# Optimization experiments

Measured on AMD Instinct MI355X. Metric: run time of the kernel, lower is better.

The kernel has to match this reference:

```python
import jax, jax.numpy as jnp
import numpy as np
import math
from jax import lax

B, HS, WS, C, T, TD, HH, TOPM = 8, 64, 64, 512, 77, 512, 8, 3
DH = C // HH
CONF_TH = 0.35


def _layernorm(x, w, b, eps=1e-5):
    mu = x.mean(-1, keepdims=True)
    var = ((x - mu) ** 2).mean(-1, keepdims=True)
    return (x - mu) * lax.rsqrt(var + eps) * w + b


def _l2norm(x, eps=1e-6):
    n = jnp.sqrt((x * x).sum(-1, keepdims=True))
    return x / jnp.maximum(n, eps)


def _forward(visual_features, text_features, geo_mask,
             ln1_w, ln1_b, wq, bq, wk, bk, wv, bv, wo, bo,
             gate_w, gate_b, logit_scale, alpha,
             ln2_w, ln2_b, ffn_w1, ffn_b1, ffn_w2, ffn_b2):
    Bb, Hs, Ws, Cv = visual_features.shape
    N = Hs * Ws
    # Pre-LN + flatten spatial
    x = _layernorm(visual_features, ln1_w, ln1_b).reshape(Bb, N, Cv)
    q_full = x @ wq + bq                                  # [B,N,C]
    pad_mask = jnp.abs(text_features).sum(-1) <= 1e-6     # [B,T]
    k_full = text_features @ wk + bk                      # [B,T,C]
    v_full = text_features @ wv + bv
    # per-token L2 normalize over full channel dim, then split heads
    q = _l2norm(q_full).reshape(Bb, N, HH, DH)
    k = _l2norm(k_full).reshape(Bb, T, HH, DH)
    v = v_full.reshape(Bb, T, HH, DH)
    scale = jnp.exp(jnp.clip(logit_scale, -2.0, 2.0)) / jnp.sqrt(jnp.float32(DH))
    sim = jnp.einsum('bnhd,bthd->bnht', q, k) * scale     # [B,N,H,T]
    # geo gate (4D tensor branch): log-bias on logits + multiplicative channel gate later
    gate_map = jnp.clip(geo_mask, 0.3, 1.0)               # [B,1,Hs,Ws]
    geo_gate_flat = gate_map.reshape(Bb, N, 1)            # [B,N,1]
    sim = sim + jnp.log(jnp.maximum(gate_map.reshape(Bb, N), 1e-6))[:, :, None, None]
    sim = jnp.where(pad_mask[:, None, None, :], -jnp.inf, sim)
    # Top-K sparsification before softmax (threshold at the K-th value)
    topv = lax.top_k(sim, TOPM)[0]                        # [B,N,H,K]
    sim = jnp.where(sim >= topv[..., -1:], sim, -jnp.inf)
    attn = jax.nn.softmax(sim, axis=-1)
    attn = attn / jnp.maximum(attn.sum(-1, keepdims=True), 1e-6)
    # fully-padded rows -> zero
    all_pad = pad_mask.all(axis=1)
    attn = jnp.where(all_pad[:, None, None, None], 0.0, attn)
    # confidence bypass: conf = max_prob * (1 - normalized entropy), mean over heads
    a_hn = attn.transpose(0, 2, 1, 3)                     # [B,H,N,T]
    maxp = a_hn.max(-1, keepdims=True)
    t_eff = jnp.maximum((a_hn > 0).astype(a_hn.dtype).sum(-1, keepdims=True), 2.0)
    p = jnp.maximum(a_hn, 1e-8)
    ent = jnp.maximum(-(p * jnp.log(p)).sum(-1, keepdims=True) / jnp.log(t_eff), 0.0)
    conf = jnp.clip(maxp * (1.0 - ent), 0.0, 1.0).mean(axis=1)   # [B,N,1]
    conf_scale = CONF_TH + (1.0 - CONF_TH) * jnp.clip(conf, 0.0, 1.0)
    aligned = jnp.einsum('bnht,bthd->bnhd', attn, v).reshape(Bb, N, HH * DH)
    aligned = (aligned @ wo + bo) * conf_scale
    gate = jax.nn.sigmoid(x @ gate_w + gate_b) * geo_gate_flat
    y = x + alpha * gate * aligned
    h = _layernorm(y, ln2_w, ln2_b)
    y = y + (jax.nn.gelu(h @ ffn_w1 + ffn_b1, approximate=False) @ ffn_w2 + ffn_b2)
    return y.reshape(Bb, Hs, Ws, Cv)


def setup_inputs() -> dict:
    key = jax.random.key(0)
    ks = jax.random.split(key, 16)
    def w(k, shp, fan_in):
        return (jax.random.normal(k, shp, jnp.float32) * (1.0 / math.sqrt(fan_in))).astype(jnp.float32)
    return {
        'visual_features': jax.random.normal(ks[0], (B, HS, WS, C), jnp.float32),
        'text_features':   jax.random.normal(ks[1], (B, T, TD), jnp.float32),
        'geo_mask':        jax.random.uniform(ks[2], (B, 1, HS, WS), jnp.float32),
        'ln1_w': jnp.ones((C,), jnp.float32), 'ln1_b': jnp.zeros((C,), jnp.float32),
        'wq': w(ks[3], (C, C), C),   'bq': jnp.zeros((C,), jnp.float32),
        'wk': w(ks[4], (TD, C), TD), 'bk': jnp.zeros((C,), jnp.float32),
        'wv': w(ks[5], (TD, C), TD), 'bv': jnp.zeros((C,), jnp.float32),
        'wo': w(ks[6], (C, C), C),   'bo': jnp.zeros((C,), jnp.float32),
        'gate_w': w(ks[7], (C, C), C), 'gate_b': jnp.zeros((C,), jnp.float32),
        'logit_scale': jnp.float32(math.log(1.0 / 0.07)),
        'alpha': jnp.float32(0.1),
        'ln2_w': jnp.ones((C,), jnp.float32), 'ln2_b': jnp.zeros((C,), jnp.float32),
        'ffn_w1': w(ks[8], (C, 4 * C), C),    'ffn_b1': jnp.zeros((4 * C,), jnp.float32),
        'ffn_w2': w(ks[9], (4 * C, C), 4 * C), 'ffn_b2': jnp.zeros((C,), jnp.float32),
    }


def reference(visual_features, text_features, geo_mask,
              ln1_w, ln1_b, wq, bq, wk, bk, wv, bv, wo, bo,
              gate_w, gate_b, logit_scale, alpha,
              ln2_w, ln2_b, ffn_w1, ffn_b1, ffn_w2, ffn_b2):
    return _forward(visual_features, text_features, geo_mask,
                    ln1_w, ln1_b, wq, bq, wk, bk, wv, bv, wo, bo,
                    gate_w, gate_b, logit_scale, alpha,
                    ln2_w, ln2_b, ffn_w1, ffn_b1, ffn_w2, ffn_b2)
```

## Files before the change

### kernel.cpp

```cpp
#include <hip/hip_runtime.h>
#include <hip/hip_bf16.h>
#include <math.h>

#define TT 77
#define MTOT 32768

typedef __attribute__((ext_vector_type(8))) short bf16x8;
typedef __attribute__((ext_vector_type(4))) float floatx4;

#define GPTR(p) ((const __attribute__((address_space(1))) void*)(p))
#define LPTR(p) ((__attribute__((address_space(3))) void*)(p))

__device__ __forceinline__ float wred_sum(float v) {
#pragma unroll
  for (int o = 32; o >= 1; o >>= 1) v += __shfl_xor(v, o, 64);
  return v;
}

__device__ __forceinline__ unsigned short f2bf(float f) {
  unsigned int u = __float_as_uint(f);
  unsigned int r = (u + 0x7fffu + ((u >> 16) & 1u)) >> 16;
  return (unsigned short)r;
}
__device__ __forceinline__ float bf2f(unsigned short h) {
  return __uint_as_float(((unsigned int)h) << 16);
}
__device__ __forceinline__ unsigned int cvt2bf(float a, float b) {
  unsigned int r;
  asm("v_cvt_pk_bf16_f32 %0, %1, %2" : "=v"(r) : "v"(a), "v"(b));
  return r;
}

__device__ __forceinline__ float fast_gelu(float o) {
  const float z = fabsf(o) * 0.70710678118654752f;
  const float t = __builtin_amdgcn_rcpf(fmaf(0.3275911f, z, 1.0f));
  float p = fmaf(1.061405429f, t, -1.453152027f);
  p = fmaf(p, t, 1.421413741f);
  p = fmaf(p, t, -0.284496736f);
  p = fmaf(p, t, 0.254829592f);
  p = p * t;
  const float erfz = fmaf(-p, __expf(-z * z), 1.0f);
  const float s = __builtin_copysignf(erfz, o);
  return 0.5f * o * (1.0f + s);
}

__device__ __forceinline__ float fast_sigmoid(float o) {
  return __builtin_amdgcn_rcpf(1.0f + __expf(-o));
}

__global__ __launch_bounds__(256)
void ln_bf16_kernel(const float* __restrict__ in, const float* __restrict__ gw,
                    const float* __restrict__ gb, unsigned short* __restrict__ out) {
  const int wv = threadIdx.x >> 6, lane = threadIdx.x & 63;
  const size_t row = (size_t)blockIdx.x * 4 + wv;
  const float* p = in + row * 512 + lane * 8;
  float4 a = *(const float4*)p;
  float4 b = *(const float4*)(p + 4);
  float s = a.x + a.y + a.z + a.w + b.x + b.y + b.z + b.w;
  float mu = wred_sum(s) * (1.0f / 512.0f);
  float d[8] = {a.x - mu, a.y - mu, a.z - mu, a.w - mu,
                b.x - mu, b.y - mu, b.z - mu, b.w - mu};
  float ss = 0.f;
#pragma unroll
  for (int i = 0; i < 8; ++i) ss = fmaf(d[i], d[i], ss);
  float var = wred_sum(ss) * (1.0f / 512.0f);
  float rstd = rsqrtf(var + 1e-5f);
  float4 w0 = *(const float4*)(gw + lane * 8);
  float4 w1 = *(const float4*)(gw + lane * 8 + 4);
  float4 c0 = *(const float4*)(gb + lane * 8);
  float4 c1 = *(const float4*)(gb + lane * 8 + 4);
  float o[8];
  o[0] = d[0] * rstd * w0.x + c0.x;  o[1] = d[1] * rstd * w0.y + c0.y;
  o[2] = d[2] * rstd * w0.z + c0.z;  o[3] = d[3] * rstd * w0.w + c0.w;
  o[4] = d[4] * rstd * w1.x + c1.x;  o[5] = d[5] * rstd * w1.y + c1.y;
  o[6] = d[6] * rstd * w1.z + c1.z;  o[7] = d[7] * rstd * w1.w + c1.w;
  __align__(16) unsigned short ob[8];
#pragma unroll
  for (int i = 0; i < 8; ++i) ob[i] = f2bf(o[i]);
  *(uint4*)(out + row * 512 + lane * 8) = *(const uint4*)ob;
}

__global__ __launch_bounds__(256)
void zero_ss_kernel(float* __restrict__ ssq) {
  ssq[blockIdx.x * 256 + threadIdx.x] = 0.0f;
}

__global__ __launch_bounds__(256)
void transpose_bf16_kernel(const float* __restrict__ W, unsigned short* __restrict__ WTb,
                           int K, int N) {
  __shared__ float s[32][33];
  const int tx = threadIdx.x & 31, ty = threadIdx.x >> 5;
  const int n0 = blockIdx.x * 32, k0 = blockIdx.y * 32;
#pragma unroll
  for (int j = 0; j < 4; ++j)
    s[ty + 8 * j][tx] = W[(size_t)(k0 + ty + 8 * j) * N + n0 + tx];
  __syncthreads();
#pragma unroll
  for (int j = 0; j < 4; ++j)
    WTb[(size_t)(n0 + ty + 8 * j) * K + k0 + tx] = f2bf(s[tx][ty + 8 * j]);
}

__global__ __launch_bounds__(256)
void transpose_pair_kernel(const float* __restrict__ W,
                           unsigned short* __restrict__ WTh,
                           unsigned short* __restrict__ WTl, int K, int N) {
  __shared__ float s[32][33];
  const int tx = threadIdx.x & 31, ty = threadIdx.x >> 5;
  const int n0 = blockIdx.x * 32, k0 = blockIdx.y * 32;
#pragma unroll
  for (int j = 0; j < 4; ++j)
    s[ty + 8 * j][tx] = W[(size_t)(k0 + ty + 8 * j) * N + n0 + tx];
  __syncthreads();
#pragma unroll
  for (int j = 0; j < 4; ++j) {
    const float a = s[tx][ty + 8 * j];
    const unsigned short hi = f2bf(a);
    WTh[(size_t)(n0 + ty + 8 * j) * K + k0 + tx] = hi;
    WTl[(size_t)(n0 + ty + 8 * j) * K + k0 + tx] = f2bf(a - bf2f(hi));
  }
}

__global__ __launch_bounds__(256)
void text_cvt_kernel(const float* __restrict__ text,
                     unsigned short* __restrict__ thi,
                     unsigned short* __restrict__ tlo,
                     float* __restrict__ negm) {
  const int wv = threadIdx.x >> 6, lane = threadIdx.x & 63;
  const int row = blockIdx.x * 4 + wv;
  if (row >= 616) {
    const uint4 z = {0u, 0u, 0u, 0u};
    *(uint4*)(thi + (size_t)row * 512 + lane * 8) = z;
    *(uint4*)(tlo + (size_t)row * 512 + lane * 8) = z;
    return;
  }
  const float* p = text + (size_t)row * 512 + lane * 8;
  float4 a = *(const float4*)p;
  float4 b = *(const float4*)(p + 4);
  float v[8] = {a.x, a.y, a.z, a.w, b.x, b.y, b.z, b.w};
  float ab = 0.f;
#pragma unroll
  for (int i = 0; i < 8; ++i) ab += fabsf(v[i]);
  ab = wred_sum(ab);
  __align__(16) unsigned short hb[8];
  __align__(16) unsigned short lb[8];
#pragma unroll
  for (int i = 0; i < 8; ++i) {
    hb[i] = f2bf(v[i]);
    lb[i] = f2bf(v[i] - bf2f(hb[i]));
  }
  *(uint4*)(thi + (size_t)row * 512 + lane * 8) = *(const uint4*)hb;
  *(uint4*)(tlo + (size_t)row * 512 + lane * 8) = *(const uint4*)lb;
  if (lane == 0) {
    const int bb = row / 77, t = row - bb * 77;
    negm[bb * 80 + t] = (ab <= 1e-6f) ? -INFINITY : 0.0f;
  }
}

__global__ __launch_bounds__(256)
void kv_gemm(const unsigned short* __restrict__ AH,
             const unsigned short* __restrict__ AL,
             const unsigned short* __restrict__ BH,
             const unsigned short* __restrict__ BL,
             const float* __restrict__ bk, const float* __restrict__ bv,
             float* __restrict__ outp) {
  const int K = 512;
  __shared__ __align__(16) unsigned short AsH[128 * 32];
  __shared__ __align__(16) unsigned short AsL[128 * 32];
  __shared__ __align__(16) unsigned short BsH[128 * 32];
  __shared__ __align__(16) unsigned short BsL[128 * 32];
  const int tid = threadIdx.x;
  const int wid = tid >> 6, lane = tid & 63;
  const int wr = wid >> 1, wc = wid & 1;
  const int m16 = lane & 15, quad = lane >> 4;
  const int row0 = blockIdx.y * 128, col0 = blockIdx.x * 128;

  const floatx4 zero4 = {0.f, 0.f, 0.f, 0.f};
  floatx4 acc[4][4];
#pragma unroll
  for (int i = 0; i < 4; ++i)
#pragma unroll
    for (int j = 0; j < 4; ++j) acc[i][j] = zero4;

  const int srow = tid >> 2;
  const int schunk = (tid & 3) ^ (srow & 3);
  const unsigned short* AgH = AH + (size_t)(row0 + srow) * K + schunk * 8;
  const unsigned short* AgL = AL + (size_t)(row0 + srow) * K + schunk * 8;
  const unsigned short* BgH = BH + (size_t)(col0 + srow) * K + schunk * 8;
  const unsigned short* BgL = BL + (size_t)(col0 + srow) * K + schunk * 8;
  char* AsHB = (char*)AsH + tid * 16;
  char* AsLB = (char*)AsL + tid * 16;
  char* BsHB = (char*)BsH + tid * 16;
  char* BsLB = (char*)BsL + tid * 16;
  const int rq = quad ^ (m16 & 3);
  const int aOfs = (wr * 64 + m16) * 32 + rq * 8;
  const int bOfs = (wc * 64 + m16) * 32 + rq * 8;

  for (int k0 = 0; k0 < K; k0 += 32) {
    __syncthreads();
    __builtin_amdgcn_global_load_lds(GPTR(AgH + k0), LPTR(AsHB), 16, 0, 0);
    __builtin_amdgcn_global_load_lds(GPTR(AgH + (size_t)64 * K + k0), LPTR(AsHB + 4096), 16, 0, 0);
    __builtin_amdgcn_global_load_lds(GPTR(AgL + k0), LPTR(AsLB), 16, 0, 0);
    __builtin_amdgcn_global_load_lds(GPTR(AgL + (size_t)64 * K + k0), LPTR(AsLB + 4096), 16, 0, 0);
    __builtin_amdgcn_global_load_lds(GPTR(BgH + k0), LPTR(BsHB), 16, 0, 0);
    __builtin_amdgcn_global_load_lds(GPTR(BgH + (size_t)64 * K + k0), LPTR(BsHB + 4096), 16, 0, 0);
    __builtin_amdgcn_global_load_lds(GPTR(BgL + k0), LPTR(BsLB), 16, 0, 0);
    __builtin_amdgcn_global_load_lds(GPTR(BgL + (size_t)64 * K + k0), LPTR(BsLB + 4096), 16, 0, 0);
    __syncthreads();
    bf16x8 afH[4], afL[4], bfH[4], bfL[4];
#pragma unroll
    for (int i = 0; i < 4; ++i) {
      afH[i] = *(const bf16x8*)(AsH + aOfs + i * 16 * 32);
      afL[i] = *(const bf16x8*)(AsL + aOfs + i * 16 * 32);
      bfH[i] = *(const bf16x8*)(BsH + bOfs + i * 16 * 32);
      bfL[i] = *(const bf16x8*)(BsL + bOfs + i * 16 * 32);
    }
#pragma unroll
    for (int mi = 0; mi < 4; ++mi)
#pragma unroll
      for (int ni = 0; ni < 4; ++ni) {
        acc[mi][ni] = __builtin_amdgcn_mfma_f32_16x16x32_bf16(afH[mi], bfH[ni], acc[mi][ni], 0, 0, 0);
        acc[mi][ni] = __builtin_amdgcn_mfma_f32_16x16x32_bf16(afH[mi], bfL[ni], acc[mi][ni], 0, 0, 0);
        acc[mi][ni] = __builtin_amdgcn_mfma_f32_16x16x32_bf16(afL[mi], bfH[ni], acc[mi][ni], 0, 0, 0);
      }
  }

  const float* bp = (col0 < 512) ? bk : bv;
  const int cbase = (col0 < 512) ? col0 : col0 - 512;
  float bb[4];
#pragma unroll
  for (int ni = 0; ni < 4; ++ni) bb[ni] = bp[cbase + wc * 64 + ni * 16 + m16];
#pragma unroll
  for (int mi = 0; mi < 4; ++mi)
#pragma unroll
    for (int r = 0; r < 4; ++r) {
      const int row = row0 + wr * 64 + mi * 16 + quad * 4 + r;
#pragma unroll
      for (int ni = 0; ni < 4; ++ni) {
        const int col = col0 + wc * 64 + ni * 16 + m16;
        outp[(size_t)row * 1024 + col] = acc[mi][ni][r] + bb[ni];
      }
    }
}

__global__ __launch_bounds__(256)
void knorm_kernel(const float* __restrict__ KV,
                  unsigned short* __restrict__ khb) {
  const int wv = threadIdx.x >> 6, lane = threadIdx.x & 63;
  const int row = blockIdx.x * 4 + wv;
  const float* p = KV + (size_t)row * 1024 + lane * 8;
  float4 a = *(const float4*)p;
  float4 b = *(const float4*)(p + 4);
  float v[8] = {a.x, a.y, a.z, a.w, b.x, b.y, b.z, b.w};
  float ss = 0.f;
#pragma unroll
  for (int i = 0; i < 8; ++i) ss = fmaf(v[i], v[i], ss);
  ss = wred_sum(ss);
  const float sc = 1.0f / fmaxf(sqrtf(ss), 1e-6f);
  const int bb = row / 77, t = row - bb * 77;
  const int c = lane * 8, h = c >> 6, d = c & 63;
  __align__(16) unsigned short ob[8];
#pragma unroll
  for (int i = 0; i < 8; ++i) ob[i] = f2bf(v[i] * sc);
  *(uint4*)(khb + (((size_t)bb * 8 + h) * 80 + t) * 64 + d) = *(const uint4*)ob;
}

__global__ __launch_bounds__(256)
void kpad_zero_kernel(unsigned short* __restrict__ khb, float* __restrict__ negm) {
  const int i = blockIdx.x * 256 + threadIdx.x;
  const int bh = i / 192, rem = i - bh * 192;
  const int t = 77 + rem / 64, d = rem & 63;
  khb[(((size_t)bh) * 80 + t) * 64 + d] = 0;
  if (i < 24) negm[(i / 3) * 80 + 77 + (i % 3)] = -INFINITY;
}

__global__ __launch_bounds__(256)
void sim_kernel(const unsigned short* __restrict__ qnb,
                const unsigned short* __restrict__ khb,
                const float* __restrict__ negm,
                const float* __restrict__ ssq,
                const float* __restrict__ logit_scale,
                float* __restrict__ SIM) {
  __shared__ __align__(16) unsigned short As[128 * 72];
  __shared__ __align__(16) unsigned short Bs[80 * 72];
  const int bh = blockIdx.y;
  const int b = bh >> 3, h = bh & 7;
  const int row0 = blockIdx.x * 128;
  const int tid = threadIdx.x;
  {
    const int r = tid >> 1, half = tid & 1;
    const unsigned short* src = qnb + ((size_t)b * 4096 + row0 + r) * 512 + h * 64 + half * 32;
    unsigned short* dst = As + r * 72 + half * 32;
    *(uint4*)dst = *(const uint4*)src;
    *(uint4*)(dst + 8) = *(const uint4*)(src + 8);
    *(uint4*)(dst + 16) = *(const uint4*)(src + 16);
    *(uint4*)(dst + 24) = *(const uint4*)(src + 24);
  }
  if (tid < 160) {
    const int r = tid >> 1, half = tid & 1;
    const unsigned short* src = khb + ((size_t)bh * 80 + r) * 64 + half * 32;
    unsigned short* dst = Bs + r * 72 + half * 32;
    *(uint4*)dst = *(const uint4*)src;
    *(uint4*)(dst + 8) = *(const uint4*)(src + 8);
    *(uint4*)(dst + 16) = *(const uint4*)(src + 16);
    *(uint4*)(dst + 24) = *(const uint4*)(src + 24);
  }
  __syncthreads();
  const int w = tid >> 6, lane = tid & 63;
  const int m16 = lane & 15, quad = lane >> 4;
  const unsigned short* aBase = As + (w * 32 + m16) * 72 + quad * 8;
  const unsigned short* bBase = Bs + m16 * 72 + quad * 8;
  bf16x8 af[2][2], bf[5][2];
#pragma unroll
  for (int mi = 0; mi < 2; ++mi)
#pragma unroll
    for (int kk = 0; kk < 2; ++kk)
      af[mi][kk] = *(const bf16x8*)(aBase + mi * 16 * 72 + kk * 32);
#pragma unroll
  for (int ni = 0; ni < 5; ++ni)
#pragma unroll
    for (int kk = 0; kk < 2; ++kk)
      bf[ni][kk] = *(const bf16x8*)(bBase + ni * 16 * 72 + kk * 32);
  const floatx4 zero4 = {0.f, 0.f, 0.f, 0.f};
  floatx4 acc[2][5];
#pragma unroll
  for (int mi = 0; mi < 2; ++mi)
#pragma unroll
    for (int ni = 0; ni < 5; ++ni) acc[mi][ni] = zero4;
#pragma unroll
  for (int kk = 0; kk < 2; ++kk)
#pragma unroll
    for (int mi = 0; mi < 2; ++mi)
#pragma unroll
      for (int ni = 0; ni < 5; ++ni)
        acc[mi][ni] = __builtin_amdgcn_mfma_f32_16x16x32_bf16(af[mi][kk], bf[ni][kk], acc[mi][ni], 0, 0, 0);
  const float ls = fminf(fmaxf(logit_scale[0], -2.0f), 2.0f);
  const float scale = expf(ls) * 0.125f;
  float nm[5];
#pragma unroll
  for (int ni = 0; ni < 5; ++ni) nm[ni] = negm[b * 80 + ni * 16 + m16];
  float* obase = SIM + ((size_t)b * 4096 + row0 + w * 32 + quad * 4) * 640 + h * 4 + (m16 & 3);
  const int jb = m16 >> 2;
#pragma unroll
  for (int mi = 0; mi < 2; ++mi)
#pragma unroll
    for (int r = 0; r < 4; ++r) {
      const int rl = row0 + w * 32 + quad * 4 + mi * 16 + r;
      const float ssv = ssq[(size_t)b * 4096 + rl];
      const float nsc = scale / fmaxf(sqrtf(ssv), 1e-6f);
#pragma unroll
      for (int ni = 0; ni < 5; ++ni)
        obase[(size_t)(mi * 16 + r) * 640 + (ni * 4 + jb) * 32] = acc[mi][ni][r] * nsc + nm[ni];
    }
}

__global__ __launch_bounds__(256)
void attn_topk_pv_kernel(const float* __restrict__ SIM,
                         const float* __restrict__ vf,
                         unsigned short* __restrict__ alignedb,
                         float* __restrict__ conf_out) {
  const int g = blockIdx.x * 256 + threadIdx.x;
  const int b = g >> 15;
  const int local = g & 32767;
  const int n = local >> 3, h = local & 7;
  const float* sp = SIM + ((size_t)b * 4096 + n) * 640 + h * 4;

  float m1 = -INFINITY, m2 = -INFINITY, m3 = -INFINITY, m4 = -INFINITY;
  int a1 = 0, a2 = 0, a3 = 0;
#pragma unroll
  for (int i = 0; i < 20; ++i) {
    const float4 q = *(const float4*)(sp + i * 32);
#pragma unroll
    for (int j = 0; j < 4; ++j) {
      const float v = (j == 0) ? q.x : (j == 1) ? q.y : (j == 2) ? q.z : q.w;
      const int t = i * 4 + j;
      const bool c1 = v > m1, c2 = v > m2, c3 = v > m3, c4 = v > m4;
      m4 = c4 ? (c3 ? m3 : v) : m4;
      m3 = c3 ? (c2 ? m2 : v) : m3;
      a3 = c3 ? (c2 ? a2 : t) : a3;
      m2 = c2 ? (c1 ? m1 : v) : m2;
      a2 = c2 ? (c1 ? a1 : t) : a2;
      m1 = c1 ? v : m1;
      a1 = c1 ? t : a1;
    }
  }

  const bool dead = (m1 == -INFINITY);
  if (dead) m1 = 0.0f;
  const bool tie = (!dead) && ((m1 == m2) || (m2 == m3) || (m3 == m4));

  const float d2 = m2 - m1, d3 = m3 - m1;
  const float e2 = __expf(d2), e3 = __expf(d3);
  float s0 = 1.0f + e2 + e3;
  float s1 = ((e2 > 0.f) ? e2 * d2 : 0.f) + ((e3 > 0.f) ? e3 * d3 : 0.f);
  float cntf = 1.0f + ((e2 > 0.f) ? 1.f : 0.f) + ((e3 > 0.f) ? 1.f : 0.f);

  unsigned short* op = alignedb + ((size_t)b * 4096 + n) * 512 + h * 64;

  if (__any(tie)) {
    if (tie) {
      s0 = 0.f; s1 = 0.f; cntf = 0.f;
      float4 acc[16];
#pragma unroll
      for (int i = 0; i < 16; ++i) acc[i] = (float4){0.f, 0.f, 0.f, 0.f};
      for (int t = 0; t < 80; ++t) {
        const float v = sp[(t >> 2) * 32 + (t & 3)];
        if (v >= m3) {
          const float e = expf(v - m1);
          if (e > 0.f) {
            s0 += e; s1 = fmaf(e, v - m1, s1); cntf += 1.f;
            const float4* vp = (const float4*)(vf + (size_t)(b * 77 + t) * 1024 + h * 64);
#pragma unroll
            for (int i = 0; i < 16; ++i) {
              const float4 x = vp[i];
              acc[i].x = fmaf(e, x.x, acc[i].x);
              acc[i].y = fmaf(e, x.y, acc[i].y);
              acc[i].z = fmaf(e, x.z, acc[i].z);
              acc[i].w = fmaf(e, x.w, acc[i].w);
            }
          }
        }
      }
      const float invt = 1.0f / s0;
#pragma unroll
      for (int i = 0; i < 8; ++i) {
        const float4 lo = acc[2 * i], hi = acc[2 * i + 1];
        uint4 pk;
        pk.x = cvt2bf(lo.x * invt, lo.y * invt);
        pk.y = cvt2bf(lo.z * invt, lo.w * invt);
        pk.z = cvt2bf(hi.x * invt, hi.y * invt);
        pk.w = cvt2bf(hi.z * invt, hi.w * invt);
        *(uint4*)(op + i * 8) = pk;
      }
    }
  }

  const float inv = 1.0f / s0;
  const float entn = (__logf(s0) - s1 * inv) + (77.0f - cntf) * 1.8420681e-7f;
  const float ent = fmaxf(entn / __logf(fmaxf(cntf, 2.0f)), 0.0f);
  float conf_h = fminf(fmaxf(inv * (1.0f - ent), 0.0f), 1.0f);
  if (dead) conf_h = 0.f;
  float cs = conf_h;
  cs += __shfl_xor(cs, 1, 64);
  cs += __shfl_xor(cs, 2, 64);
  cs += __shfl_xor(cs, 4, 64);
  if (h == 0) {
    const float cm = fminf(fmaxf(cs * 0.125f, 0.0f), 1.0f);
    conf_out[(size_t)b * 4096 + n] = 0.35f + 0.65f * cm;
  }

  if (!tie) {
    const float wA = dead ? 0.f : inv;
    const float wB = e2 * inv, wC = e3 * inv;
    const float* v1p = vf + (size_t)(b * 77 + a1) * 1024 + h * 64;
    const float* v2p = vf + (size_t)(b * 77 + a2) * 1024 + h * 64;
    const float* v3p = vf + (size_t)(b * 77 + a3) * 1024 + h * 64;
#pragma unroll
    for (int i = 0; i < 8; ++i) {
      const float4 a0 = ((const float4*)v1p)[2 * i];
      const float4 a1v = ((const float4*)v1p)[2 * i + 1];
      const float4 b0 = ((const float4*)v2p)[2 * i];
      const float4 b1 = ((const float4*)v2p)[2 * i + 1];
      const float4 c0 = ((const float4*)v3p)[2 * i];
      const float4 c1 = ((const float4*)v3p)[2 * i + 1];
      float4 r0, r1;
      r0.x = fmaf(wC, c0.x, fmaf(wB, b0.x, wA * a0.x));
      r0.y = fmaf(wC, c0.y, fmaf(wB, b0.y, wA * a0.y));
      r0.z = fmaf(wC, c0.z, fmaf(wB, b0.z, wA * a0.z));
      r0.w = fmaf(wC, c0.w, fmaf(wB, b0.w, wA * a0.w));
      r1.x = fmaf(wC, c1.x, fmaf(wB, b1.x, wA * a1v.x));
      r1.y = fmaf(wC, c1.y, fmaf(wB, b1.y, wA * a1v.y));
      r1.z = fmaf(wC, c1.z, fmaf(wB, b1.z, wA * a1v.z));
      r1.w = fmaf(wC, c1.w, fmaf(wB, b1.w, wA * a1v.w));
      uint4 pk;
      pk.x = cvt2bf(r0.x, r0.y);
      pk.y = cvt2bf(r0.z, r0.w);
      pk.z = cvt2bf(r1.x, r1.y);
      pk.w = cvt2bf(r1.z, r1.w);
      *(uint4*)(op + i * 8) = pk;
    }
  }
}

template <int EPI, int KC>
__global__ __launch_bounds__(256)
void mfma_gemm(const unsigned short* __restrict__ A,
               const unsigned short* __restrict__ WT,
               const float* __restrict__ bias,
               void* __restrict__ outv, int M, int N,
               const unsigned short* __restrict__ e0b,
               const float* __restrict__ e1f,
               const float* __restrict__ e2f,
               const float* __restrict__ scf) {
  __shared__ __align__(16) unsigned short As[128 * 32];
  __shared__ __align__(16) unsigned short Bs[128 * 32];
  const int tid = threadIdx.x;
  const int wid = tid >> 6, lane = tid & 63;
  const int wr = wid >> 1, wc = wid & 1;
  const int m16 = lane & 15, quad = lane >> 4;

  const int nwg = gridDim.x * gridDim.y;
  const int orig = blockIdx.y * gridDim.x + blockIdx.x;
  const int qq = nwg >> 3, rr = nwg & 7;
  const int xcd = orig & 7, base = orig >> 3;
  const int logical = (xcd < rr ? xcd * (qq + 1) : rr * (qq + 1) + (xcd - rr) * qq) + base;
  const int bx = logical % gridDim.x, by = logical / gridDim.x;
  const int row0 = by * 128, col0 = bx * 128;

  const floatx4 zero4 = {0.f, 0.f, 0.f, 0.f};
  floatx4 acc[4][4];
#pragma unroll
  for (int i = 0; i < 4; ++i)
#pragma unroll
    for (int j = 0; j < 4; ++j) acc[i][j] = zero4;

  const int srow = tid >> 2;
  const int schunk = (tid & 3) ^ (srow & 3);
  const unsigned short* Ag = A + (size_t)(row0 + srow) * KC + schunk * 8;
  const unsigned short* Bg = WT + (size_t)(col0 + srow) * KC + schunk * 8;
  char* AsB = (char*)As + tid * 16;
  char* BsB = (char*)Bs + tid * 16;
  const int rq = quad ^ (m16 & 3);
  const unsigned short* aP = As + (wr * 64 + m16) * 32 + rq * 8;
  const unsigned short* bP = Bs + (wc * 64 + m16) * 32 + rq * 8;

  for (int k0 = 0; k0 < KC; k0 += 32) {
    __syncthreads();
    __builtin_amdgcn_global_load_lds(GPTR(Ag + k0), LPTR(AsB), 16, 0, 0);
    __builtin_amdgcn_global_load_lds(GPTR(Ag + (size_t)64 * KC + k0), LPTR(AsB + 4096), 16, 0, 0);
    __builtin_amdgcn_global_load_lds(GPTR(Bg + k0), LPTR(BsB), 16, 0, 0);
    __builtin_amdgcn_global_load_lds(GPTR(Bg + (size_t)64 * KC + k0), LPTR(BsB + 4096), 16, 0, 0);
    __syncthreads();
    bf16x8 af[4], bfr[4];
#pragma unroll
    for (int i = 0; i < 4; ++i) {
      af[i] = *(const bf16x8*)(aP + i * 16 * 32);
      bfr[i] = *(const bf16x8*)(bP + i * 16 * 32);
    }
#pragma unroll
    for (int mi = 0; mi < 4; ++mi)
#pragma unroll
      for (int ni = 0; ni < 4; ++ni)
        acc[mi][ni] = __builtin_amdgcn_mfma_f32_16x16x32_bf16(af[mi], bfr[ni], acc[mi][ni], 0, 0, 0);
  }

  float* outf = (float*)outv;
  unsigned short* outb = (unsigned short*)outv;
  const unsigned short* albf = (const unsigned short*)e1f;
  float bb[4];
#pragma unroll
  for (int ni = 0; ni < 4; ++ni) bb[ni] = bias[col0 + wc * 64 + ni * 16 + m16];
  const float alphav = (EPI == 2) ? scf[0] : 0.f;

#pragma unroll
  for (int mi = 0; mi < 4; ++mi) {
#pragma unroll
    for (int r = 0; r < 4; ++r) {
      const int row = row0 + wr * 64 + mi * 16 + quad * 4 + r;
      float o[4];
#pragma unroll
      for (int ni = 0; ni < 4; ++ni) o[ni] = acc[mi][ni][r] + bb[ni];
      const size_t basei = (size_t)row * N + col0 + wc * 64 + m16;

      if (EPI == 5) {
        const unsigned int p01 = cvt2bf(o[0], o[1]);
        const unsigned int p23 = cvt2bf(o[2], o[3]);
        outb[basei] = (unsigned short)p01;
        outb[basei + 16] = (unsigned short)(p01 >> 16);
        outb[basei + 32] = (unsigned short)p23;
        outb[basei + 48] = (unsigned short)(p23 >> 16);
        float p = fmaf(o[0], o[0], fmaf(o[1], o[1], fmaf(o[2], o[2], o[3] * o[3])));
        p += __shfl_xor(p, 1, 64);
        p += __shfl_xor(p, 2, 64);
        p += __shfl_xor(p, 4, 64);
        p += __shfl_xor(p, 8, 64);
        if (m16 == 0) atomicAdd(const_cast<float*>(e1f) + row, p);
      } else if (EPI == 3) {
        const unsigned int p01 = cvt2bf(fast_gelu(o[0]), fast_gelu(o[1]));
        const unsigned int p23 = cvt2bf(fast_gelu(o[2]), fast_gelu(o[3]));
        outb[basei] = (unsigned short)p01;
        outb[basei + 16] = (unsigned short)(p01 >> 16);
        outb[basei + 32] = (unsigned short)p23;
        outb[basei + 48] = (unsigned short)(p23 >> 16);
      } else if (EPI == 1) {
        const float rowscale = e1f[row];
        const unsigned int p01 = cvt2bf(o[0] * rowscale, o[1] * rowscale);
        const unsigned int p23 = cvt2bf(o[2] * rowscale, o[3] * rowscale);
        outb[basei] = (unsigned short)p01;
        outb[basei + 16] = (unsigned short)(p01 >> 16);
        outb[basei + 32] = (unsigned short)p23;
        outb[basei + 48] = (unsigned short)(p23 >> 16);
      } else if (EPI == 2) {
        const float geo = fminf(fmaxf(e2f[row], 0.3f), 1.0f);
#pragma unroll
        for (int ni = 0; ni < 4; ++ni) {
          const size_t idx = basei + ni * 16;
          const float x = bf2f(e0b[idx]);
          const float al = bf2f(albf[idx]);
          const float sg = fast_sigmoid(o[ni]);
          outf[idx] = x + alphav * sg * geo * al;
        }
      } else {
#pragma unroll
        for (int ni = 0; ni < 4; ++ni) {
          const size_t idx = basei + ni * 16;
          outf[idx] = o[ni] + e1f[idx];
        }
      }
    }
  }
}

extern "C" void kernel_launch(void* const* d_in, const int* in_sizes, int n_in,
                              void* d_out, int out_size, void* d_ws, size_t ws_size,
                              hipStream_t stream) {
  const float* visual = (const float*)d_in[0];
  const float* text   = (const float*)d_in[1];
  const float* geo    = (const float*)d_in[2];
  const float* ln1_w  = (const float*)d_in[3];
  const float* ln1_b  = (const float*)d_in[4];
  const float* wq     = (const float*)d_in[5];
  const float* bq     = (const float*)d_in[6];
  const float* wk     = (const float*)d_in[7];
  const float* bk     = (const float*)d_in[8];
  const float* wvw    = (const float*)d_in[9];
  const float* bv     = (const float*)d_in[10];
  const float* wo     = (const float*)d_in[11];
  const float* bo     = (const float*)d_in[12];
  const float* gate_w = (const float*)d_in[13];
  const float* gate_b = (const float*)d_in[14];
  const float* logit_scale = (const float*)d_in[15];
  const float* alpha  = (const float*)d_in[16];
  const float* ln2_w  = (const float*)d_in[17];
  const float* ln2_b  = (const float*)d_in[18];
  const float* ffn_w1 = (const float*)d_in[19];
  const float* ffn_b1 = (const float*)d_in[20];
  const float* ffn_w2 = (const float*)d_in[21];
  const float* ffn_b2 = (const float*)d_in[22];
  float* out = (float*)d_out;

  char* ws = (char*)d_ws;
  float* R0            = (float*)ws;
  float* BUF2          = (float*)(ws + 88080384);
  unsigned short* Xb   = (unsigned short*)(ws + 155189248);
  unsigned short* QNb  = (unsigned short*)(ws + 188743680);
  unsigned short* wqT  = (unsigned short*)(ws + 222298112);
  unsigned short* woT  = wqT + 262144;
  unsigned short* gateT = woT + 262144;
  unsigned short* w1T  = gateT + 262144;
  unsigned short* w2T  = w1T + 1048576;
  unsigned short* KHb  = w2T + 1048576;
  float* NEGM = (float*)(ws + 230146048);
  float* CONF = (float*)(ws + 230148608);
  float* SSQ  = (float*)(ws + 230279680);

  float* KV            = (float*)(ws + 88080384);
  unsigned short* THi  = (unsigned short*)(ws + 88080384 + 2621440);
  unsigned short* TLo  = THi + 640 * 512;
  unsigned short* WKVh = TLo + 640 * 512;
  unsigned short* WKVl = WKVh + 1024 * 512;

  float* SIM = R0;
  unsigned short* ALb = QNb;

  transpose_bf16_kernel<<<dim3(16, 16), 256, 0, stream>>>(wq, wqT, 512, 512);
  transpose_bf16_kernel<<<dim3(16, 16), 256, 0, stream>>>(wo, woT, 512, 512);
  transpose_bf16_kernel<<<dim3(16, 16), 256, 0, stream>>>(gate_w, gateT, 512, 512);
  transpose_bf16_kernel<<<dim3(64, 16), 256, 0, stream>>>(ffn_w1, w1T, 512, 2048);
  transpose_bf16_kernel<<<dim3(16, 64), 256, 0, stream>>>(ffn_w2, w2T, 2048, 512);
  transpose_pair_kernel<<<dim3(16, 16), 256, 0, stream>>>(wk, WKVh, WKVl, 512, 512);
  transpose_pair_kernel<<<dim3(16, 16), 256, 0, stream>>>(wvw, WKVh + 512 * 512, WKVl + 512 * 512, 512, 512);

  ln_bf16_kernel<<<MTOT / 4, 256, 0, stream>>>(visual, ln1_w, ln1_b, Xb);
  zero_ss_kernel<<<128, 256, 0, stream>>>(SSQ);
  text_cvt_kernel<<<160, 256, 0, stream>>>(text, THi, TLo, NEGM);
  kv_gemm<<<dim3(8, 5), 256, 0, stream>>>(THi, TLo, WKVh, WKVl, bk, bv, KV);
  knorm_kernel<<<154, 256, 0, stream>>>(KV, KHb);
  kpad_zero_kernel<<<48, 256, 0, stream>>>(KHb, NEGM);
  mfma_gemm<5, 512><<<dim3(4, 256), 256, 0, stream>>>(Xb, wqT, bq, QNb, MTOT, 512,
                                                      nullptr, SSQ, nullptr, nullptr);
  sim_kernel<<<dim3(32, 64), 256, 0, stream>>>(QNb, KHb, NEGM, SSQ, logit_scale, SIM);
  attn_topk_pv_kernel<<<1024, 256, 0, stream>>>(SIM, KV + 512, ALb, CONF);
  unsigned short* AOb = (unsigned short*)R0;
  mfma_gemm<1, 512><<<dim3(4, 256), 256, 0, stream>>>(ALb, woT, bo, AOb, MTOT, 512,
                                                      nullptr, CONF, nullptr, nullptr);
  mfma_gemm<2, 512><<<dim3(4, 256), 256, 0, stream>>>(Xb, gateT, gate_b, BUF2, MTOT, 512,
                                                      Xb, (const float*)AOb, geo, alpha);
  ln_bf16_kernel<<<MTOT / 4, 256, 0, stream>>>(BUF2, ln2_w, ln2_b, Xb);
  unsigned short* GCH = (unsigned short*)R0;
  for (int ch = 0; ch < 2; ++ch) {
    const size_t off = (size_t)ch * 16384;
    mfma_gemm<3, 512><<<dim3(16, 128), 256, 0, stream>>>(Xb + off * 512, w1T, ffn_b1, GCH,
                                                         16384, 2048,
                                                         nullptr, nullptr, nullptr, nullptr);
    mfma_gemm<4, 2048><<<dim3(4, 128), 256, 0, stream>>>(GCH, w2T, ffn_b2, out + off * 512,
                                                         16384, 512,
                                                         nullptr, BUF2 + off * 512, nullptr, nullptr);
  }
}
```

Before: 616.9 us.

## Fuse similarity GEMM with top-k softmax and PV into one kernel

The similarity MFMA kernel now keeps its per-tile logits in shared memory instead of writing a large fp32 SIM tensor to global memory. The same block then runs the top-3 selection, softmax weights and value gather, with two threads splitting each row's 64 head channels. Per-head confidence is accumulated with atomicAdd into a buffer zeroed up front, and the final 0.35+0.65*clamp mapping moves into the output-projection GEMM epilogue. This removes the SIM round-trip through global memory and one kernel launch. In exchange it adds atomics, redundant top-k scans done by both half-threads, and more shared memory per block.

```diff
diff --git a/kernel.cpp b/kernel.cpp
--- a/kernel.cpp
+++ b/kernel.cpp
@@ -81,8 +81,10 @@
 }
 
 __global__ __launch_bounds__(256)
-void zero_ss_kernel(float* __restrict__ ssq) {
-  ssq[blockIdx.x * 256 + threadIdx.x] = 0.0f;
+void zero_acc_kernel(float* __restrict__ ssq, float* __restrict__ conf) {
+  const int i = blockIdx.x * 256 + threadIdx.x;
+  ssq[i] = 0.0f;
+  conf[i] = 0.0f;
 }
 
 __global__ __launch_bounds__(256)
@@ -274,18 +276,24 @@
 }
 
 __global__ __launch_bounds__(256)
-void sim_kernel(const unsigned short* __restrict__ qnb,
-                const unsigned short* __restrict__ khb,
-                const float* __restrict__ negm,
-                const float* __restrict__ ssq,
-                const float* __restrict__ logit_scale,
-                float* __restrict__ SIM) {
-  __shared__ __align__(16) unsigned short As[128 * 72];
-  __shared__ __align__(16) unsigned short Bs[80 * 72];
+void sim_attn_kernel(const unsigned short* __restrict__ qnb,
+                     const unsigned short* __restrict__ khb,
+                     const float* __restrict__ negm,
+                     const float* __restrict__ ssq,
+                     const float* __restrict__ logit_scale,
+                     const float* __restrict__ vf,
+                     unsigned short* __restrict__ alignedb,
+                     float* __restrict__ confacc) {
+  __shared__ __align__(16) char lbuf[128 * 81 * 4];
+  unsigned short* As = (unsigned short*)lbuf;
+  unsigned short* Bs = As + 128 * 72;
+  float* simt = (float*)lbuf;
+
   const int bh = blockIdx.y;
   const int b = bh >> 3, h = bh & 7;
   const int row0 = blockIdx.x * 128;
   const int tid = threadIdx.x;
+
   {
     const int r = tid >> 1, half = tid & 1;
     const unsigned short* src = qnb + ((size_t)b * 4096 + row0 + r) * 512 + h * 64 + half * 32;
@@ -305,6 +313,7 @@
     *(uint4*)(dst + 24) = *(const uint4*)(src + 24);
   }
   __syncthreads();
+
   const int w = tid >> 6, lane = tid & 63;
   const int m16 = lane & 15, quad = lane >> 4;
   const unsigned short* aBase = As + (w * 32 + m16) * 72 + quad * 8;
@@ -320,6 +329,8 @@
 #pragma unroll
     for (int kk = 0; kk < 2; ++kk)
       bf[ni][kk] = *(const bf16x8*)(bBase + ni * 16 * 72 + kk * 32);
+  __syncthreads();
+
   const floatx4 zero4 = {0.f, 0.f, 0.f, 0.f};
   floatx4 acc[2][5];
 #pragma unroll
@@ -333,55 +344,41 @@
 #pragma unroll
       for (int ni = 0; ni < 5; ++ni)
         acc[mi][ni] = __builtin_amdgcn_mfma_f32_16x16x32_bf16(af[mi][kk], bf[ni][kk], acc[mi][ni], 0, 0, 0);
+
   const float ls = fminf(fmaxf(logit_scale[0], -2.0f), 2.0f);
   const float scale = expf(ls) * 0.125f;
   float nm[5];
 #pragma unroll
   for (int ni = 0; ni < 5; ++ni) nm[ni] = negm[b * 80 + ni * 16 + m16];
-  float* obase = SIM + ((size_t)b * 4096 + row0 + w * 32 + quad * 4) * 640 + h * 4 + (m16 & 3);
-  const int jb = m16 >> 2;
 #pragma unroll
   for (int mi = 0; mi < 2; ++mi)
 #pragma unroll
     for (int r = 0; r < 4; ++r) {
-      const int rl = row0 + w * 32 + quad * 4 + mi * 16 + r;
-      const float ssv = ssq[(size_t)b * 4096 + rl];
+      const int lr = w * 32 + quad * 4 + mi * 16 + r;
+      const float ssv = ssq[(size_t)b * 4096 + row0 + lr];
       const float nsc = scale / fmaxf(sqrtf(ssv), 1e-6f);
 #pragma unroll
       for (int ni = 0; ni < 5; ++ni)
-        obase[(size_t)(mi * 16 + r) * 640 + (ni * 4 + jb) * 32] = acc[mi][ni][r] * nsc + nm[ni];
-    }
-}
-
-__global__ __launch_bounds__(256)
-void attn_topk_pv_kernel(const float* __restrict__ SIM,
-                         const float* __restrict__ vf,
-                         unsigned short* __restrict__ alignedb,
-                         float* __restrict__ conf_out) {
-  const int g = blockIdx.x * 256 + threadIdx.x;
-  const int b = g >> 15;
-  const int local = g & 32767;
-  const int n = local >> 3, h = local & 7;
-  const float* sp = SIM + ((size_t)b * 4096 + n) * 640 + h * 4;
+        simt[lr * 81 + ni * 16 + m16] = acc[mi][ni][r] * nsc + nm[ni];
+    }
+  __syncthreads();
+
+  const int lr = tid >> 1, half = tid & 1;
+  const int n = row0 + lr;
+  const float* sp = simt + lr * 81;
 
   float m1 = -INFINITY, m2 = -INFINITY, m3 = -INFINITY, m4 = -INFINITY;
   int a1 = 0, a2 = 0, a3 = 0;
-#pragma unroll
-  for (int i = 0; i < 20; ++i) {
-    const float4 q = *(const float4*)(sp + i * 32);
-#pragma unroll
-    for (int j = 0; j < 4; ++j) {
-      const float v = (j == 0) ? q.x : (j == 1) ? q.y : (j == 2) ? q.z : q.w;
-      const int t = i * 4 + j;
-      const bool c1 = v > m1, c2 = v > m2, c3 = v > m3, c4 = v > m4;
-      m4 = c4 ? (c3 ? m3 : v) : m4;
-      m3 = c3 ? (c2 ? m2 : v) : m3;
-      a3 = c3 ? (c2 ? a2 : t) : a3;
-      m2 = c2 ? (c1 ? m1 : v) : m2;
-      a2 = c2 ? (c1 ? a1 : t) : a2;
-      m1 = c1 ? v : m1;
-      a1 = c1 ? t : a1;
-    }
+  for (int t = 0; t < 80; ++t) {
+    const float v = sp[t];
+    const bool c1 = v > m1, c2 = v > m2, c3 = v > m3, c4 = v > m4;
+    m4 = c4 ? (c3 ? m3 : v) : m4;
+    m3 = c3 ? (c2 ? m2 : v) : m3;
+    a3 = c3 ? (c2 ? a2 : t) : a3;
+    m2 = c2 ? (c1 ? m1 : v) : m2;
+    a2 = c2 ? (c1 ? a1 : t) : a2;
+    m1 = c1 ? v : m1;
+    a1 = c1 ? t : a1;
   }
 
   const bool dead = (m1 == -INFINITY);
@@ -394,83 +391,66 @@
   float s1 = ((e2 > 0.f) ? e2 * d2 : 0.f) + ((e3 > 0.f) ? e3 * d3 : 0.f);
   float cntf = 1.0f + ((e2 > 0.f) ? 1.f : 0.f) + ((e3 > 0.f) ? 1.f : 0.f);
 
-  unsigned short* op = alignedb + ((size_t)b * 4096 + n) * 512 + h * 64;
-
-  if (__any(tie)) {
-    if (tie) {
-      s0 = 0.f; s1 = 0.f; cntf = 0.f;
-      float4 acc[16];
-#pragma unroll
-      for (int i = 0; i < 16; ++i) acc[i] = (float4){0.f, 0.f, 0.f, 0.f};
-      for (int t = 0; t < 80; ++t) {
-        const float v = sp[(t >> 2) * 32 + (t & 3)];
-        if (v >= m3) {
-          const float e = expf(v - m1);
-          if (e > 0.f) {
-            s0 += e; s1 = fmaf(e, v - m1, s1); cntf += 1.f;
-            const float4* vp = (const float4*)(vf + (size_t)(b * 77 + t) * 1024 + h * 64);
-#pragma unroll
-            for (int i = 0; i < 16; ++i) {
-              const float4 x = vp[i];
-              acc[i].x = fmaf(e, x.x, acc[i].x);
-              acc[i].y = fmaf(e, x.y, acc[i].y);
-              acc[i].z = fmaf(e, x.z, acc[i].z);
-              acc[i].w = fmaf(e, x.w, acc[i].w);
-            }
+  unsigned short* op = alignedb + ((size_t)b * 4096 + n) * 512 + h * 64 + half * 32;
+
+  if (tie) {
+    s0 = 0.f; s1 = 0.f; cntf = 0.f;
+    float4 acc2[8];
+#pragma unroll
+    for (int i = 0; i < 8; ++i) acc2[i] = (float4){0.f, 0.f, 0.f, 0.f};
+    for (int t = 0; t < 80; ++t) {
+      const float v = sp[t];
+      if (v >= m3) {
+        const float e = expf(v - m1);
+        if (e > 0.f) {
+          s0 += e; s1 = fmaf(e, v - m1, s1); cntf += 1.f;
+          const float4* vp = (const float4*)(vf + (size_t)(b * 77 + t) * 1024 + h * 64 + half * 32);
+#pragma unroll
+          for (int i = 0; i < 8; ++i) {
+            const float4 x = vp[i];
+            acc2[i].x = fmaf(e, x.x, acc2[i].x);
+            acc2[i].y = fmaf(e, x.y, acc2[i].y);
+            acc2[i].z = fmaf(e, x.z, acc2[i].z);
+            acc2[i].w = fmaf(e, x.w, acc2[i].w);
           }
         }
       }
-      const float invt = 1.0f / s0;
-#pragma unroll
-      for (int i = 0; i < 8; ++i) {
-        const float4 lo = acc[2 * i], hi = acc[2 * i + 1];
-        uint4 pk;
-        pk.x = cvt2bf(lo.x * invt, lo.y * invt);
-        pk.y = cvt2bf(lo.z * invt, lo.w * invt);
-        pk.z = cvt2bf(hi.x * invt, hi.y * invt);
-        pk.w = cvt2bf(hi.z * invt, hi.w * invt);
-        *(uint4*)(op + i * 8) = pk;
-      }
-    }
-  }
-
-  const float inv = 1.0f / s0;
-  const float entn = (__logf(s0) - s1 * inv) + (77.0f - cntf) * 1.8420681e-7f;
-  const float ent = fmaxf(entn / __logf(fmaxf(cntf, 2.0f)), 0.0f);
-  float conf_h = fminf(fmaxf(inv * (1.0f - ent), 0.0f), 1.0f);
-  if (dead) conf_h = 0.f;
-  float cs = conf_h;
-  cs += __shfl_xor(cs, 1, 64);
-  cs += __shfl_xor(cs, 2, 64);
-  cs += __shfl_xor(cs, 4, 64);
-  if (h == 0) {
-    const float cm = fminf(fmaxf(cs * 0.125f, 0.0f), 1.0f);
-    conf_out[(size_t)b * 4096 + n] = 0.35f + 0.65f * cm;
-  }
-
-  if (!tie) {
-    const float wA = dead ? 0.f : inv;
-    const float wB = e2 * inv, wC = e3 * inv;
-    const float* v1p = vf + (size_t)(b * 77 + a1) * 1024 + h * 64;
-    const float* v2p = vf + (size_t)(b * 77 + a2) * 1024 + h * 64;
-    const float* v3p = vf + (size_t)(b * 77 + a3) * 1024 + h * 64;
-#pragma unroll
-    for (int i = 0; i < 8; ++i) {
-      const float4 a0 = ((const float4*)v1p)[2 * i];
-      const float4 a1v = ((const float4*)v1p)[2 * i + 1];
-      const float4 b0 = ((const float4*)v2p)[2 * i];
-      const float4 b1 = ((const float4*)v2p)[2 * i + 1];
-      const float4 c0 = ((const float4*)v3p)[2 * i];
-      const float4 c1 = ((const float4*)v3p)[2 * i + 1];
+    }
+    const float invt = 1.0f / s0;
+#pragma unroll
+    for (int i = 0; i < 4; ++i) {
+      const float4 lo = acc2[2 * i], hi = acc2[2 * i + 1];
+      uint4 pk;
+      pk.x = cvt2bf(lo.x * invt, lo.y * invt);
+      pk.y = cvt2bf(lo.z * invt, lo.w * invt);
+      pk.z = cvt2bf(hi.x * invt, hi.y * invt);
+      pk.w = cvt2bf(hi.z * invt, hi.w * invt);
+      *(uint4*)(op + i * 8) = pk;
+    }
+  } else {
+    const float inv0 = 1.0f / s0;
+    const float wA = dead ? 0.f : inv0;
+    const float wB = e2 * inv0, wC = e3 * inv0;
+    const float* v1p = vf + (size_t)(b * 77 + a1) * 1024 + h * 64 + half * 32;
+    const float* v2p = vf + (size_t)(b * 77 + a2) * 1024 + h * 64 + half * 32;
+    const float* v3p = vf + (size_t)(b * 77 + a3) * 1024 + h * 64 + half * 32;
+#pragma unroll
+    for (int i = 0; i < 4; ++i) {
+      const float4 x0 = ((const float4*)v1p)[2 * i];
+      const float4 x1 = ((const float4*)v1p)[2 * i + 1];
+      const float4 y0 = ((const float4*)v2p)[2 * i];
+      const float4 y1 = ((const float4*)v2p)[2 * i + 1];
+      const float4 z0 = ((const float4*)v3p)[2 * i];
+      const float4 z1 = ((const float4*)v3p)[2 * i + 1];
       float4 r0, r1;
-      r0.x = fmaf(wC, c0.x, fmaf(wB, b0.x, wA * a0.x));
-      r0.y = fmaf(wC, c0.y, fmaf(wB, b0.y, wA * a0.y));
-      r0.z = fmaf(wC, c0.z, fmaf(wB, b0.z, wA * a0.z));
-      r0.w = fmaf(wC, c0.w, fmaf(wB, b0.w, wA * a0.w));
-      r1.x = fmaf(wC, c1.x, fmaf(wB, b1.x, wA * a1v.x));
-      r1.y = fmaf(wC, c1.y, fmaf(wB, b1.y, wA * a1v.y));
-      r1.z = fmaf(wC, c1.z, fmaf(wB, b1.z, wA * a1v.z));
-      r1.w = fmaf(wC, c1.w, fmaf(wB, b1.w, wA * a1v.w));
+      r0.x = fmaf(wC, z0.x, fmaf(wB, y0.x, wA * x0.x));
+      r0.y = fmaf(wC, z0.y, fmaf(wB, y0.y, wA * x0.y));
+      r0.z = fmaf(wC, z0.z, fmaf(wB, y0.z, wA * x0.z));
+      r0.w = fmaf(wC, z0.w, fmaf(wB, y0.w, wA * x0.w));
+      r1.x = fmaf(wC, z1.x, fmaf(wB, y1.x, wA * x1.x));
+      r1.y = fmaf(wC, z1.y, fmaf(wB, y1.y, wA * x1.y));
+      r1.z = fmaf(wC, z1.z, fmaf(wB, y1.z, wA * x1.z));
+      r1.w = fmaf(wC, z1.w, fmaf(wB, y1.w, wA * x1.w));
       uint4 pk;
       pk.x = cvt2bf(r0.x, r0.y);
       pk.y = cvt2bf(r0.z, r0.w);
@@ -478,6 +458,15 @@
       pk.w = cvt2bf(r1.z, r1.w);
       *(uint4*)(op + i * 8) = pk;
     }
+  }
+
+  if (half == 0) {
+    const float inv = 1.0f / s0;
+    const float entn = (__logf(s0) - s1 * inv) + (77.0f - cntf) * 1.8420681e-7f;
+    const float ent = fmaxf(entn / __logf(fmaxf(cntf, 2.0f)), 0.0f);
+    float conf_h = fminf(fmaxf(inv * (1.0f - ent), 0.0f), 1.0f);
+    if (dead) conf_h = 0.f;
+    atomicAdd(confacc + (size_t)b * 4096 + n, conf_h * 0.125f);
   }
 }
 
@@ -582,7 +571,8 @@
         outb[basei + 32] = (unsigned short)p23;
         outb[basei + 48] = (unsigned short)(p23 >> 16);
       } else if (EPI == 1) {
-        const float rowscale = e1f[row];
+        const float cm = fminf(fmaxf(e1f[row], 0.0f), 1.0f);
+        const float rowscale = 0.35f + 0.65f * cm;
         const unsigned int p01 = cvt2bf(o[0] * rowscale, o[1] * rowscale);
         const unsigned int p23 = cvt2bf(o[2] * rowscale, o[3] * rowscale);
         outb[basei] = (unsigned short)p01;
@@ -659,8 +649,8 @@
   unsigned short* WKVh = TLo + 640 * 512;
   unsigned short* WKVl = WKVh + 1024 * 512;
 
-  float* SIM = R0;
-  unsigned short* ALb = QNb;
+  unsigned short* ALb = (unsigned short*)R0;
+  unsigned short* AOb = QNb;
 
   transpose_bf16_kernel<<<dim3(16, 16), 256, 0, stream>>>(wq, wqT, 512, 512);
   transpose_bf16_kernel<<<dim3(16, 16), 256, 0, stream>>>(wo, woT, 512, 512);
@@ -671,16 +661,15 @@
   transpose_pair_kernel<<<dim3(16, 16), 256, 0, stream>>>(wvw, WKVh + 512 * 512, WKVl + 512 * 512, 512, 512);
 
   ln_bf16_kernel<<<MTOT / 4, 256, 0, stream>>>(visual, ln1_w, ln1_b, Xb);
-  zero_ss_kernel<<<128, 256, 0, stream>>>(SSQ);
+  zero_acc_kernel<<<128, 256, 0, stream>>>(SSQ, CONF);
   text_cvt_kernel<<<160, 256, 0, stream>>>(text, THi, TLo, NEGM);
   kv_gemm<<<dim3(8, 5), 256, 0, stream>>>(THi, TLo, WKVh, WKVl, bk, bv, KV);
   knorm_kernel<<<154, 256, 0, stream>>>(KV, KHb);
   kpad_zero_kernel<<<48, 256, 0, stream>>>(KHb, NEGM);
   mfma_gemm<5, 512><<<dim3(4, 256), 256, 0, stream>>>(Xb, wqT, bq, QNb, MTOT, 512,
                                                       nullptr, SSQ, nullptr, nullptr);
-  sim_kernel<<<dim3(32, 64), 256, 0, stream>>>(QNb, KHb, NEGM, SSQ, logit_scale, SIM);
-  attn_topk_pv_kernel<<<1024, 256, 0, stream>>>(SIM, KV + 512, ALb, CONF);
-  unsigned short* AOb = (unsigned short*)R0;
+  sim_attn_kernel<<<dim3(32, 64), 256, 0, stream>>>(QNb, KHb, NEGM, SSQ, logit_scale,
+                                                    KV + 512, ALb, CONF);
   mfma_gemm<1, 512><<<dim3(4, 256), 256, 0, stream>>>(ALb, woT, bo, AOb, MTOT, 512,
                                                       nullptr, CONF, nullptr, nullptr);
   mfma_gemm<2, 512><<<dim3(4, 256), 256, 0, stream>>>(Xb, gateT, gate_b, BUF2, MTOT, 512,
```

New measurement: 583.4 us. -5.4%, faster.
